# Kernel tuning notes

Hardware: AMD Instinct MI355X
Metric: run time of the kernel (lower is better)

## Reference

```python
import jax, jax.numpy as jnp
import numpy as np
from jax import lax

N, T, V, E, H, D, B = 16384, 16, 10000, 256, 256, 512, 128


def setup_inputs() -> dict:
    key = jax.random.key(0)
    ks = jax.random.split(key, 12)
    tok = jax.random.randint(ks[0], (N, T), 1, V)
    lens = jax.random.randint(ks[1], (N,), 4, T + 1)
    tok = jnp.where(jnp.arange(T)[None, :] < lens[:, None], tok, 0)  # pad_id = 0
    ast_path_len = jnp.full((B,), N // B, dtype=jnp.int32)  # 128 paths per sample
    u = lambda k, s: jax.random.uniform(k, s, jnp.float32, -0.1, 0.1)
    emb = u(ks[2], (V, E)).at[0].set(0.0)  # padding_idx=0 row zeroed
    return {
        "ast_path": tok,
        "ast_path_len": ast_path_len,
        "emb": emb,
        "W_ih_f": u(ks[3], (4 * H, E)), "W_hh_f": u(ks[4], (4 * H, H)), "b_f": u(ks[5], (4 * H,)),
        "W_ih_b": u(ks[6], (4 * H, E)), "W_hh_b": u(ks[7], (4 * H, H)), "b_b": u(ks[8], (4 * H,)),
        "W_lin": u(ks[9], (D, 2 * H)), "b_lin": jnp.zeros((D,), jnp.float32),
    }


def _lstm_final_h(x_tm, lens, W_ih, W_hh, b, reverse):
    # x_tm: [T, N, E]; returns final hidden state [N, H] honoring per-seq length
    n = x_tm.shape[1]
    h0 = jnp.zeros((n, H), x_tm.dtype)

    def step(carry, xt):
        h, c = carry
        x, t = xt
        gates = x @ W_ih.T + h @ W_hh.T + b  # [N, 4H]
        i, f, g, o = jnp.split(gates, 4, axis=-1)
        c_new = jax.nn.sigmoid(f) * c + jax.nn.sigmoid(i) * jnp.tanh(g)
        h_new = jax.nn.sigmoid(o) * jnp.tanh(c_new)
        m = (t < lens)[:, None]  # packed-sequence semantics: frozen past length
        return (jnp.where(m, h_new, h), jnp.where(m, c_new, c)), None

    (h, _), _ = lax.scan(step, (h0, h0), (x_tm, jnp.arange(x_tm.shape[0])), reverse=reverse)
    return h


def reference(ast_path, ast_path_len, emb, W_ih_f, W_hh_f, b_f, W_ih_b, W_hh_b, b_b, W_lin, b_lin):
    lens = (ast_path != 0).sum(axis=-1)  # pad_id = 0
    x = emb[ast_path]                     # [N, T, E]; dropout is identity at eval
    x_tm = jnp.swapaxes(x, 0, 1)          # [T, N, E]
    h_fwd = _lstm_final_h(x_tm, lens, W_ih_f, W_hh_f, b_f, reverse=False)
    h_bwd = _lstm_final_h(x_tm, lens, W_ih_b, W_hh_b, b_b, reverse=True)
    h_n = jnp.concatenate([h_fwd, h_bwd], axis=1)        # [N, 2H]
    repr_ = h_n @ W_lin.T + b_lin                         # [N, D]
    # segment-mean pooling over path groups (replaces the Python loop)
    n_paths = repr_.shape[0]
    seg_ids = jnp.repeat(jnp.arange(ast_path_len.shape[0]), ast_path_len,
                         total_repeat_length=n_paths)
    sums = jax.ops.segment_sum(repr_, seg_ids, num_segments=ast_path_len.shape[0])
    pooled = sums / ast_path_len[:, None].astype(repr_.dtype)  # [B, D]
    norm = jnp.sqrt(jnp.sum(pooled * pooled, axis=-1, keepdims=True))
    return pooled / jnp.maximum(norm, 1e-5)
```

## Files before the change

### kernel.cpp

```cpp
#include <hip/hip_runtime.h>
#include <stdint.h>

#define N_SEQ 16384
#define T_LEN 16
#define E_DIM 256
#define H_DIM 256
#define K_DIM 512
#define B_SAMP 128
#define V_SIZE 10000
#define NBLK_LENS (N_SEQ / 256)

typedef __bf16 bf16x8 __attribute__((ext_vector_type(8)));
typedef float  f32x4  __attribute__((ext_vector_type(4)));
typedef unsigned short ush;

__device__ __forceinline__ ush f2bf(float x) {
  unsigned int u = __float_as_uint(x);
  u = (u + 0x7fffu + ((u >> 16) & 1u)) >> 16;
  return (ush)u;
}
__device__ __forceinline__ float bf2f(ush v) {
  return __uint_as_float(((unsigned int)v) << 16);
}
__device__ __forceinline__ float sigmoidf_(float x) {
  return 1.0f / (1.0f + __expf(-x));
}
__device__ __forceinline__ float tanhf_(float x) {
  float e = __expf(2.0f * x);
  return 1.0f - 2.0f / (e + 1.0f);
}
__device__ __forceinline__ void glds16(const void* g, const void* l) {
  __builtin_amdgcn_global_load_lds(
      (const __attribute__((address_space(1))) unsigned int*)g,
      (__attribute__((address_space(3))) unsigned int*)l, 16, 0, 0);
}


__global__ __launch_bounds__(256) void k_lens(const int* __restrict__ tok, int* __restrict__ lens,
                                              int* __restrict__ blockhist) {
  __shared__ int lh[17];
  if (threadIdx.x < 17) lh[threadIdx.x] = 0;
  __syncthreads();
  int n = blockIdx.x * 256 + threadIdx.x;
  const int* r = tok + n * T_LEN;
  int c = 0;
#pragma unroll
  for (int t = 0; t < T_LEN; ++t) c += (r[t] != 0);
  lens[n] = c;
  atomicAdd(&lh[c], 1);
  __syncthreads();
  if (threadIdx.x < 17) blockhist[blockIdx.x * 17 + threadIdx.x] = lh[threadIdx.x];
}

__global__ void k_offsets(const int* __restrict__ blockhist, int* __restrict__ base,
                          int* __restrict__ cnts) {
  if (threadIdx.x == 0) {
    int tot[17];
    for (int l = 0; l <= 16; ++l) {
      int s = 0;
      for (int b = 0; b < NBLK_LENS; ++b) s += blockhist[b * 17 + l];
      tot[l] = s;
    }
    int start[17];
    int off = 0;
    for (int l = 16; l >= 0; --l) { start[l] = off; off += tot[l]; }
    for (int l = 0; l <= 16; ++l) {
      int run = start[l];
      for (int b = 0; b < NBLK_LENS; ++b) { base[b * 17 + l] = run; run += blockhist[b * 17 + l]; }
    }
    for (int t = 0; t < 16; ++t) {
      int c = 0;
      for (int l = t + 1; l <= 16; ++l) c += tot[l];
      cnts[t] = c;
    }
  }
}

__global__ __launch_bounds__(256) void k_scatter(const int* __restrict__ lens, const int* __restrict__ base,
                                                 int* __restrict__ perm, int* __restrict__ pinv,
                                                 int* __restrict__ plens) {
  __shared__ int lh[17];
  if (threadIdx.x < 17) lh[threadIdx.x] = 0;
  __syncthreads();
  int n = blockIdx.x * 256 + threadIdx.x;
  int l = lens[n];
  int lr = atomicAdd(&lh[l], 1);
  int pos = base[blockIdx.x * 17 + l] + lr;
  perm[pos] = n;
  pinv[n] = pos;
  plens[pos] = l;
}

__global__ __launch_bounds__(256) void k_tokperm(const int* __restrict__ tok, const int* __restrict__ perm,
                                                 int* __restrict__ tokperm) {
  int id = blockIdx.x * 256 + threadIdx.x;
  int t = id >> 14;
  int pos = id & (N_SEQ - 1);
  tokperm[id] = tok[perm[pos] * T_LEN + t];
}

__global__ __launch_bounds__(256) void k_embcvt(const float* __restrict__ emb, ush* __restrict__ out) {
  int i = blockIdx.x * 256 + threadIdx.x;
  out[i] = f2bf(emb[i]);
}

__global__ __launch_bounds__(256) void k_wprep(const float* __restrict__ Wih_f, const float* __restrict__ Whh_f,
                                               const float* __restrict__ Wih_b, const float* __restrict__ Whh_b,
                                               ush* __restrict__ wpt_f, ush* __restrict__ wpt_b) {
  int id = blockIdx.x * 256 + threadIdx.x;
  int dir = id >> 19;
  int rem = id & ((1 << 19) - 1);
  int p = rem >> 9;
  int k = rem & 511;
  int nb = p >> 8, wc = (p >> 6) & 3, q = (p >> 4) & 3, jj = p & 15;
  int r = q * 256 + nb * 64 + wc * 16 + jj;
  const float* Wih = dir ? Wih_b : Wih_f;
  const float* Whh = dir ? Whh_b : Whh_f;
  float v = (k < 256) ? Wih[r * 256 + k] : Whh[r * 256 + (k - 256)];
  ush* o = dir ? wpt_b : wpt_f;
  o[p * 512 + k] = f2bf(v);
}


__global__ __launch_bounds__(512, 4)
void k_step(const ush* __restrict__ embbf, const int* __restrict__ tokperm,
            const int* __restrict__ plens, const int* __restrict__ cnts,
            const ush* __restrict__ wpt_f, const ush* __restrict__ wpt_b,
            const float* __restrict__ bias_f, const float* __restrict__ bias_b,
            const ush* __restrict__ hr_f, ush* __restrict__ hw_f,
            const ush* __restrict__ hr_b, ush* __restrict__ hw_b,
            float* __restrict__ c_f, float* __restrict__ c_b,
            int s) {
  const int dir = blockIdx.y;
  const int t = dir ? (15 - s) : s;
  const int cnt = cnts[t];
  const int mblk = blockIdx.x >> 2;
  const int m0 = mblk * 128;
  if (m0 >= cnt) return;

  const int nblk = blockIdx.x & 3;
  const ush* wpt = dir ? wpt_b : wpt_f;
  const float* bias = dir ? bias_b : bias_f;
  const ush* hr = dir ? hr_b : hr_f;
  ush* hw = dir ? hw_b : hw_f;
  float* cc = dir ? c_b : c_f;

  __shared__ __align__(128) unsigned char ldsA[128 * 128];
  __shared__ __align__(128) unsigned char ldsB[256 * 128];

  const int tid = threadIdx.x;
  const int lane = tid & 63;
  const int w = tid >> 6;
  const int wr = w >> 2;
  const int wc = w & 3;

  const int l8 = lane >> 3;
  const int l7 = lane & 7;
  const int arow0 = 16 * w + l8;
  const int arow1 = arow0 + 8;
  const int ach0 = l7 ^ (arow0 & 7);
  const int ach1 = l7 ^ (arow1 & 7);
  const unsigned aoffE0 = (unsigned)tokperm[t * N_SEQ + m0 + arow0] * E_DIM + ach0 * 8;
  const unsigned aoffE1 = (unsigned)tokperm[t * N_SEQ + m0 + arow1] * E_DIM + ach1 * 8;
  const unsigned aoffH0 = (unsigned)(m0 + arow0) * H_DIM + ach0 * 8;
  const unsigned aoffH1 = (unsigned)(m0 + arow1) * H_DIM + ach1 * 8;
  unsigned boff[4];
#pragma unroll
  for (int jj = 0; jj < 4; ++jj) {
    const int brow = 32 * w + 8 * jj + l8;
    const int bch = l7 ^ (brow & 7);
    boff[jj] = (unsigned)(nblk * 256 + brow) * K_DIM + bch * 8;
  }

  f32x4 acc[4][4] = {};
  const int frow = lane & 15;
  const int fkq = lane >> 4;

  for (int kt = 0; kt < 8; ++kt) {
    const int k0 = kt * 64;
    if (kt < 4) {
      glds16(embbf + aoffE0 + k0, &ldsA[(16 * w) * 128]);
      glds16(embbf + aoffE1 + k0, &ldsA[(16 * w + 8) * 128]);
    } else {
      glds16(hr + aoffH0 + (k0 - E_DIM), &ldsA[(16 * w) * 128]);
      glds16(hr + aoffH1 + (k0 - E_DIM), &ldsA[(16 * w + 8) * 128]);
    }
#pragma unroll
    for (int jj = 0; jj < 4; ++jj)
      glds16(wpt + boff[jj] + k0, &ldsB[(32 * w + 8 * jj) * 128]);
    __syncthreads();
#pragma unroll
    for (int ksub = 0; ksub < 2; ++ksub) {
      bf16x8 av[4], bv[4];
#pragma unroll
      for (int fr = 0; fr < 4; ++fr) {
        const int row = wr * 64 + fr * 16 + frow;
        const int ch = (ksub * 4 + fkq) ^ (row & 7);
        av[fr] = *(const bf16x8*)&ldsA[row * 128 + ch * 16];
      }
#pragma unroll
      for (int fc = 0; fc < 4; ++fc) {
        const int row = wc * 64 + fc * 16 + frow;
        const int ch = (ksub * 4 + fkq) ^ (row & 7);
        bv[fc] = *(const bf16x8*)&ldsB[row * 128 + ch * 16];
      }
#pragma unroll
      for (int fr = 0; fr < 4; ++fr)
#pragma unroll
        for (int fc = 0; fc < 4; ++fc)
          acc[fr][fc] = __builtin_amdgcn_mfma_f32_16x16x32_bf16(av[fr], bv[fc], acc[fr][fc], 0, 0, 0);
    }
    __syncthreads();
  }

  const int j = nblk * 64 + wc * 16 + frow;
  const float b0 = bias[j], b1 = bias[256 + j], b2 = bias[512 + j], b3 = bias[768 + j];
#pragma unroll
  for (int fr = 0; fr < 4; ++fr) {
    const int n0 = m0 + wr * 64 + fr * 16 + fkq * 4;
    const int4 l4 = *(const int4*)&plens[n0];
    const f32x4 gi = acc[fr][0], gf = acc[fr][1], gg = acc[fr][2], go = acc[fr][3];
#pragma unroll
    for (int r = 0; r < 4; ++r) {
      const int lnv = (r == 0) ? l4.x : (r == 1) ? l4.y : (r == 2) ? l4.z : l4.w;
      if (t < lnv) {
        const size_t idx = (size_t)(n0 + r) * H_DIM + j;
        const float iv = sigmoidf_(gi[r] + b0);
        const float fv = sigmoidf_(gf[r] + b1);
        const float gv = tanhf_(gg[r] + b2);
        const float ov = sigmoidf_(go[r] + b3);
        const bool first = dir ? (t == lnv - 1) : (t == 0);
        const float cn = fv * (first ? 0.0f : cc[idx]) + iv * gv;
        cc[idx] = cn;
        hw[idx] = f2bf(ov * tanhf_(cn));
      }
    }
  }
}


__global__ __launch_bounds__(256) void k_pool(const ush* __restrict__ h0f, const ush* __restrict__ h1f,
                                              const ush* __restrict__ h0b,
                                              const int* __restrict__ pinv, const int* __restrict__ lens,
                                              const int* __restrict__ plen,
                                              float* __restrict__ pooled) {
  const int b = blockIdx.x, tid = threadIdx.x;
  int start = 0;
  for (int i = 0; i < b; ++i) start += plen[i];
  const int cnt = plen[b];
  float s0 = 0.f, s1 = 0.f;
  for (int r = 0; r < cnt; ++r) {
    const int n = start + r;
    const size_t pr = (size_t)pinv[n];
    const int l = lens[n];
    const ush* hf = (l & 1) ? h1f : h0f;
    s0 += bf2f(hf[pr * H_DIM + tid]);
    s1 += bf2f(h0b[pr * H_DIM + tid]);
  }
  float inv = 1.0f / (float)cnt;
  pooled[b * 512 + tid] = s0 * inv;
  pooled[b * 512 + H_DIM + tid] = s1 * inv;
}


__global__ __launch_bounds__(256) void k_final(const float* __restrict__ pooled,
                                               const float* __restrict__ W,
                                               const float* __restrict__ bl,
                                               float* __restrict__ out) {
  const int b = blockIdx.x, tid = threadIdx.x;
  __shared__ float pv[512];
  __shared__ float pre[512];
  __shared__ float red[4];
  pv[tid] = pooled[b * 512 + tid];
  pv[tid + 256] = pooled[b * 512 + 256 + tid];
  __syncthreads();
#pragma unroll
  for (int half = 0; half < 2; ++half) {
    const int dd = tid + half * 256;
    const f32x4* wr = (const f32x4*)(W + (size_t)dd * 512);
    const f32x4* pvv = (const f32x4*)pv;
    float s = bl[dd];
#pragma unroll 4
    for (int k4 = 0; k4 < 128; ++k4) {
      f32x4 wv = wr[k4], xv = pvv[k4];
      s += wv[0] * xv[0] + wv[1] * xv[1] + wv[2] * xv[2] + wv[3] * xv[3];
    }
    pre[dd] = s;
  }
  __syncthreads();
  float ss = pre[tid] * pre[tid] + pre[tid + 256] * pre[tid + 256];
#pragma unroll
  for (int off = 32; off > 0; off >>= 1) ss += __shfl_down(ss, off, 64);
  if ((tid & 63) == 0) red[tid >> 6] = ss;
  __syncthreads();
  float tot = red[0] + red[1] + red[2] + red[3];
  float scale = 1.0f / fmaxf(sqrtf(tot), 1e-5f);
  out[b * 512 + tid] = pre[tid] * scale;
  out[b * 512 + 256 + tid] = pre[tid + 256] * scale;
}


extern "C" void kernel_launch(void* const* d_in, const int* in_sizes, int n_in,
                              void* d_out, int out_size, void* d_ws, size_t ws_size,
                              hipStream_t stream) {
  const int* tok    = (const int*)d_in[0];
  const int* plen   = (const int*)d_in[1];
  const float* emb  = (const float*)d_in[2];
  const float* Wih_f = (const float*)d_in[3];
  const float* Whh_f = (const float*)d_in[4];
  const float* b_f   = (const float*)d_in[5];
  const float* Wih_b = (const float*)d_in[6];
  const float* Whh_b = (const float*)d_in[7];
  const float* b_b   = (const float*)d_in[8];
  const float* Wlin  = (const float*)d_in[9];
  const float* blin  = (const float*)d_in[10];
  float* out = (float*)d_out;

  char* ws = (char*)d_ws;
  size_t off = 0;
  auto alloc = [&](size_t bytes) {
    void* p = ws + off;
    off = (off + bytes + 255) & ~(size_t)255;
    return p;
  };
  ush* embbf   = (ush*)alloc((size_t)V_SIZE * E_DIM * 2);
  ush* wptf    = (ush*)alloc((size_t)1024 * K_DIM * 2);
  ush* wptb    = (ush*)alloc((size_t)1024 * K_DIM * 2);
  int* lens    = (int*)alloc((size_t)N_SEQ * 4);
  int* perm    = (int*)alloc((size_t)N_SEQ * 4);
  int* pinv    = (int*)alloc((size_t)N_SEQ * 4);
  int* plens   = (int*)alloc((size_t)N_SEQ * 4);
  int* tokperm = (int*)alloc((size_t)T_LEN * N_SEQ * 4);
  int* blockhist = (int*)alloc((size_t)NBLK_LENS * 17 * 4);
  int* base    = (int*)alloc((size_t)NBLK_LENS * 17 * 4);
  int* cnts    = (int*)alloc(16 * 4);
  ush* h0f     = (ush*)alloc((size_t)N_SEQ * H_DIM * 2);
  ush* h1f     = (ush*)alloc((size_t)N_SEQ * H_DIM * 2);
  ush* h0b     = (ush*)alloc((size_t)N_SEQ * H_DIM * 2);
  ush* h1b     = (ush*)alloc((size_t)N_SEQ * H_DIM * 2);
  float* cf    = (float*)alloc((size_t)N_SEQ * H_DIM * 4);
  float* cb    = (float*)alloc((size_t)N_SEQ * H_DIM * 4);
  float* pooled = (float*)alloc((size_t)B_SAMP * 512 * 4);

  hipMemsetAsync(h0f, 0, (size_t)N_SEQ * H_DIM * 2, stream);
  hipMemsetAsync(h1f, 0, (size_t)N_SEQ * H_DIM * 2, stream);
  hipMemsetAsync(h0b, 0, (size_t)N_SEQ * H_DIM * 2, stream);
  hipMemsetAsync(h1b, 0, (size_t)N_SEQ * H_DIM * 2, stream);

  k_lens<<<NBLK_LENS, 256, 0, stream>>>(tok, lens, blockhist);
  k_offsets<<<1, 64, 0, stream>>>(blockhist, base, cnts);
  k_scatter<<<NBLK_LENS, 256, 0, stream>>>(lens, base, perm, pinv, plens);
  k_tokperm<<<(T_LEN * N_SEQ) / 256, 256, 0, stream>>>(tok, perm, tokperm);
  k_embcvt<<<(V_SIZE * E_DIM) / 256, 256, 0, stream>>>(emb, embbf);
  k_wprep<<<(2 * 1024 * K_DIM) / 256, 256, 0, stream>>>(Wih_f, Whh_f, Wih_b, Whh_b, wptf, wptb);

  dim3 grid(512, 2);
  for (int s = 0; s < T_LEN; ++s) {
    const ush* hrf = (s & 1) ? h1f : h0f;
    ush* hwf       = (s & 1) ? h0f : h1f;
    const ush* hrb = (s & 1) ? h1b : h0b;
    ush* hwb       = (s & 1) ? h0b : h1b;
    k_step<<<grid, 512, 0, stream>>>(embbf, tokperm, plens, cnts, wptf, wptb,
                                     b_f, b_b, hrf, hwf, hrb, hwb, cf, cb, s);
  }
  k_pool<<<B_SAMP, 256, 0, stream>>>(h0f, h1f, h0b, pinv, lens, plen, pooled);
  k_final<<<B_SAMP, 256, 0, stream>>>(pooled, Wlin, blin, out);
}
```

Baseline: 816.8 us.

## Transpose LSTM cell state, prefetch it early, fuse pool and final kernels

The cell state is stored transposed ([H][N]), so each lane loads and stores four consecutive sequences as one f32x4 vector. Those loads are issued before the GEMM loop so their latency overlaps the MFMA work. The epilogue skips row groups whose sequences have all finished, the launch-bounds occupancy hint rises from 4 to 6, and pooling is fused with the final linear and normalise step, which removes one launch and the intermediate buffer. The cost is more live registers across the main loop, which the higher occupancy target could force to spill. The transposed c layout also means a whole 16-row wave writes to scattered 64-byte segments.

```diff
diff --git a/kernel.cpp b/kernel.cpp
--- a/kernel.cpp
+++ b/kernel.cpp
@@ -122,14 +122,14 @@
 }
 
 
-__global__ __launch_bounds__(512, 4)
+__global__ __launch_bounds__(512, 6)
 void k_step(const ush* __restrict__ embbf, const int* __restrict__ tokperm,
             const int* __restrict__ plens, const int* __restrict__ cnts,
             const ush* __restrict__ wpt_f, const ush* __restrict__ wpt_b,
             const float* __restrict__ bias_f, const float* __restrict__ bias_b,
             const ush* __restrict__ hr_f, ush* __restrict__ hw_f,
             const ush* __restrict__ hr_b, ush* __restrict__ hw_b,
-            float* __restrict__ c_f, float* __restrict__ c_b,
+            float* __restrict__ cT_f, float* __restrict__ cT_b,
             int s) {
   const int dir = blockIdx.y;
   const int t = dir ? (15 - s) : s;
@@ -143,7 +143,7 @@
   const float* bias = dir ? bias_b : bias_f;
   const ush* hr = dir ? hr_b : hr_f;
   ush* hw = dir ? hw_b : hw_f;
-  float* cc = dir ? c_b : c_f;
+  float* cT = dir ? cT_b : cT_f;
 
   __shared__ __align__(128) unsigned char ldsA[128 * 128];
   __shared__ __align__(128) unsigned char ldsB[256 * 128];
@@ -153,6 +153,19 @@
   const int w = tid >> 6;
   const int wr = w >> 2;
   const int wc = w & 3;
+  const int frow = lane & 15;
+  const int fkq = lane >> 4;
+
+  const int j = nblk * 64 + wc * 16 + frow;
+  const float b0 = bias[j], b1 = bias[256 + j], b2 = bias[512 + j], b3 = bias[768 + j];
+  int4 l4[4];
+  f32x4 cv4[4];
+#pragma unroll
+  for (int fr = 0; fr < 4; ++fr) {
+    const int n0 = m0 + wr * 64 + fr * 16 + fkq * 4;
+    l4[fr] = *(const int4*)&plens[n0];
+    cv4[fr] = *(const f32x4*)&cT[(size_t)j * N_SEQ + n0];
+  }
 
   const int l8 = lane >> 3;
   const int l7 = lane & 7;
@@ -173,8 +186,6 @@
   }
 
   f32x4 acc[4][4] = {};
-  const int frow = lane & 15;
-  const int fkq = lane >> 4;
 
   for (int kt = 0; kt < 8; ++kt) {
     const int k0 = kt * 64;
@@ -213,38 +224,43 @@
     __syncthreads();
   }
 
-  const int j = nblk * 64 + wc * 16 + frow;
-  const float b0 = bias[j], b1 = bias[256 + j], b2 = bias[512 + j], b3 = bias[768 + j];
 #pragma unroll
   for (int fr = 0; fr < 4; ++fr) {
     const int n0 = m0 + wr * 64 + fr * 16 + fkq * 4;
-    const int4 l4 = *(const int4*)&plens[n0];
+    const int4 ln = l4[fr];
+    const int lmax = max(max(ln.x, ln.y), max(ln.z, ln.w));
+    if (t >= lmax) continue;
+    f32x4 cv = cv4[fr];
     const f32x4 gi = acc[fr][0], gf = acc[fr][1], gg = acc[fr][2], go = acc[fr][3];
 #pragma unroll
     for (int r = 0; r < 4; ++r) {
-      const int lnv = (r == 0) ? l4.x : (r == 1) ? l4.y : (r == 2) ? l4.z : l4.w;
+      const int lnv = (r == 0) ? ln.x : (r == 1) ? ln.y : (r == 2) ? ln.z : ln.w;
       if (t < lnv) {
-        const size_t idx = (size_t)(n0 + r) * H_DIM + j;
         const float iv = sigmoidf_(gi[r] + b0);
         const float fv = sigmoidf_(gf[r] + b1);
         const float gv = tanhf_(gg[r] + b2);
         const float ov = sigmoidf_(go[r] + b3);
         const bool first = dir ? (t == lnv - 1) : (t == 0);
-        const float cn = fv * (first ? 0.0f : cc[idx]) + iv * gv;
-        cc[idx] = cn;
-        hw[idx] = f2bf(ov * tanhf_(cn));
+        const float cn = fv * (first ? 0.0f : cv[r]) + iv * gv;
+        cv[r] = cn;
+        hw[(size_t)(n0 + r) * H_DIM + j] = f2bf(ov * tanhf_(cn));
       }
     }
-  }
-}
-
-
-__global__ __launch_bounds__(256) void k_pool(const ush* __restrict__ h0f, const ush* __restrict__ h1f,
-                                              const ush* __restrict__ h0b,
-                                              const int* __restrict__ pinv, const int* __restrict__ lens,
-                                              const int* __restrict__ plen,
-                                              float* __restrict__ pooled) {
+    *(f32x4*)&cT[(size_t)j * N_SEQ + n0] = cv;
+  }
+}
+
+
+__global__ __launch_bounds__(256) void k_poolfinal(const ush* __restrict__ h0f, const ush* __restrict__ h1f,
+                                                   const ush* __restrict__ h0b,
+                                                   const int* __restrict__ pinv, const int* __restrict__ lens,
+                                                   const int* __restrict__ plen,
+                                                   const float* __restrict__ W, const float* __restrict__ bl,
+                                                   float* __restrict__ out) {
   const int b = blockIdx.x, tid = threadIdx.x;
+  __shared__ float pv[512];
+  __shared__ float pre[512];
+  __shared__ float red[4];
   int start = 0;
   for (int i = 0; i < b; ++i) start += plen[i];
   const int cnt = plen[b];
@@ -257,22 +273,9 @@
     s0 += bf2f(hf[pr * H_DIM + tid]);
     s1 += bf2f(h0b[pr * H_DIM + tid]);
   }
-  float inv = 1.0f / (float)cnt;
-  pooled[b * 512 + tid] = s0 * inv;
-  pooled[b * 512 + H_DIM + tid] = s1 * inv;
-}
-
-
-__global__ __launch_bounds__(256) void k_final(const float* __restrict__ pooled,
-                                               const float* __restrict__ W,
-                                               const float* __restrict__ bl,
-                                               float* __restrict__ out) {
-  const int b = blockIdx.x, tid = threadIdx.x;
-  __shared__ float pv[512];
-  __shared__ float pre[512];
-  __shared__ float red[4];
-  pv[tid] = pooled[b * 512 + tid];
-  pv[tid + 256] = pooled[b * 512 + 256 + tid];
+  const float inv = 1.0f / (float)cnt;
+  pv[tid] = s0 * inv;
+  pv[tid + 256] = s1 * inv;
   __syncthreads();
 #pragma unroll
   for (int half = 0; half < 2; ++half) {
@@ -338,9 +341,8 @@
   ush* h1f     = (ush*)alloc((size_t)N_SEQ * H_DIM * 2);
   ush* h0b     = (ush*)alloc((size_t)N_SEQ * H_DIM * 2);
   ush* h1b     = (ush*)alloc((size_t)N_SEQ * H_DIM * 2);
-  float* cf    = (float*)alloc((size_t)N_SEQ * H_DIM * 4);
-  float* cb    = (float*)alloc((size_t)N_SEQ * H_DIM * 4);
-  float* pooled = (float*)alloc((size_t)B_SAMP * 512 * 4);
+  float* cTf   = (float*)alloc((size_t)H_DIM * N_SEQ * 4);
+  float* cTb   = (float*)alloc((size_t)H_DIM * N_SEQ * 4);
 
   hipMemsetAsync(h0f, 0, (size_t)N_SEQ * H_DIM * 2, stream);
   hipMemsetAsync(h1f, 0, (size_t)N_SEQ * H_DIM * 2, stream);
@@ -361,8 +363,7 @@
     const ush* hrb = (s & 1) ? h1b : h0b;
     ush* hwb       = (s & 1) ? h0b : h1b;
     k_step<<<grid, 512, 0, stream>>>(embbf, tokperm, plens, cnts, wptf, wptb,
-                                     b_f, b_b, hrf, hwf, hrb, hwb, cf, cb, s);
-  }
-  k_pool<<<B_SAMP, 256, 0, stream>>>(h0f, h1f, h0b, pinv, lens, plen, pooled);
-  k_final<<<B_SAMP, 256, 0, stream>>>(pooled, Wlin, blin, out);
-}
+                                     b_f, b_b, hrf, hwf, hrb, hwb, cTf, cTb, s);
+  }
+  k_poolfinal<<<B_SAMP, 256, 0, stream>>>(h0f, h1f, h0b, pinv, lens, plen, Wlin, blin, out);
+}
```

Result: slower. 3.238 ms (+296.5%).
